# Optimization experiments

Hardware: AMD Instinct MI355X
Metric: run time of the kernel (lower is better)

## Reference

```python
import jax, jax.numpy as jnp
import numpy as np


def _orthogonal(key, n):
    a = jax.random.normal(key, (n, n), dtype=jnp.float32)
    q, r = jnp.linalg.qr(a)
    # sign correction as in torch.nn.init.orthogonal_
    q = q * jnp.sign(jnp.diag(r))
    return q


def setup_inputs() -> dict:
    key = jax.random.key(0)
    k_x, k_b, k_l = jax.random.split(key, 3)
    bs, seq_len, x_dim = 128, 2048, 256
    x_set = jax.random.normal(k_x, (bs, seq_len, x_dim), dtype=jnp.float32)
    B = _orthogonal(k_b, x_dim)
    Lam = _orthogonal(k_l, x_dim)
    return {"x_set": x_set, "B": B, "Lam": Lam}


def reference(x_set, B, Lam):
    # h_t = tanh(B @ x_t + Lambda @ h_{t-1}), h_0-input = 0
    # torch: bmm(B, x[:,T,None]) == x_t @ B.T for row-vector batch layout
    bs, seq_len, x_dim = x_set.shape

    def step(h, x_t):
        h_new = jnp.tanh(x_t @ B.T + h @ Lam.T)  # [bs, x_dim]
        return h_new, h_new

    h0 = jnp.zeros((bs, x_dim), dtype=x_set.dtype)
    _, hs = jax.lax.scan(step, h0, jnp.swapaxes(x_set, 0, 1))  # [T, bs, x_dim]
    return jnp.swapaxes(hs, 0, 1)  # [bs, T, x_dim]
```

## Files before the change

### kernel.cpp

```cpp
#include <hip/hip_runtime.h>

#define TT 2048
#define DD 256

typedef __fp16 half2_t __attribute__((ext_vector_type(2)));
typedef __fp16 half8_t __attribute__((ext_vector_type(8)));
typedef float f32x4_t __attribute__((ext_vector_type(4)));

static __device__ __forceinline__ float fdot2(half2_t a, half2_t b, float c) {
  return __builtin_amdgcn_fdot2(a, b, c, false);
}

static __device__ __forceinline__ float fast_tanh(float y) {
  float e = __builtin_amdgcn_exp2f(y * 2.885390081777927f);
  return 1.0f - 2.0f * __builtin_amdgcn_rcpf(e + 1.0f);
}

static __device__ __forceinline__ float dpp_xor1(float v) {
  return __builtin_bit_cast(float, __builtin_amdgcn_update_dpp(
      0, __builtin_bit_cast(int, v), 0xB1 , 0xF, 0xF, true));
}
static __device__ __forceinline__ float dpp_xor2(float v) {
  return __builtin_bit_cast(float, __builtin_amdgcn_update_dpp(
      0, __builtin_bit_cast(int, v), 0x4E , 0xF, 0xF, true));
}
static __device__ __forceinline__ float dpp_xor8(float v) {
  return __builtin_bit_cast(float, __builtin_amdgcn_update_dpp(
      0, __builtin_bit_cast(int, v), 0x128 , 0xF, 0xF, true));
}

#define BST 264
__global__ __launch_bounds__(256, 1) void rnn_u_gemm(
    const float* __restrict__ X, const float* __restrict__ Bm,
    float* __restrict__ U)
{
  extern __shared__ __fp16 bsh[];
  const int tid = threadIdx.x;

  {
    const float* br = Bm + tid * DD;
    __fp16* dst = bsh + tid * BST;
#pragma unroll
    for (int c = 0; c < 32; ++c) {
      float4 v0 = *(const float4*)(br + c * 8);
      float4 v1 = *(const float4*)(br + c * 8 + 4);
      uint4 w;
      w.x = __builtin_bit_cast(unsigned int, __builtin_amdgcn_cvt_pkrtz(v0.x, v0.y));
      w.y = __builtin_bit_cast(unsigned int, __builtin_amdgcn_cvt_pkrtz(v0.z, v0.w));
      w.z = __builtin_bit_cast(unsigned int, __builtin_amdgcn_cvt_pkrtz(v1.x, v1.y));
      w.w = __builtin_bit_cast(unsigned int, __builtin_amdgcn_cvt_pkrtz(v1.z, v1.w));
      *(uint4*)(dst + c * 8) = w;
    }
  }
  __syncthreads();

  const int wv = tid >> 6;
  const int l = tid & 63;
  const int l16 = l & 15;
  const int lk = l >> 4;
  const size_t tok0 = (size_t)blockIdx.x * 128 + wv * 32;

  f32x4_t acc[2][16];
#pragma unroll
  for (int m = 0; m < 2; ++m)
#pragma unroll
    for (int n = 0; n < 16; ++n)
      acc[m][n] = (f32x4_t){0.f, 0.f, 0.f, 0.f};

  const float* xA0 = X + (tok0 + l16) * DD + lk * 8;
  const float* xA1 = X + (tok0 + 16 + l16) * DD + lk * 8;

#pragma unroll
  for (int ks = 0; ks < 8; ++ks) {
    float4 a00 = *(const float4*)(xA0 + ks * 32);
    float4 a01 = *(const float4*)(xA0 + ks * 32 + 4);
    float4 a10 = *(const float4*)(xA1 + ks * 32);
    float4 a11 = *(const float4*)(xA1 + ks * 32 + 4);
    half2_t p0 = __builtin_amdgcn_cvt_pkrtz(a00.x, a00.y);
    half2_t p1 = __builtin_amdgcn_cvt_pkrtz(a00.z, a00.w);
    half2_t p2 = __builtin_amdgcn_cvt_pkrtz(a01.x, a01.y);
    half2_t p3 = __builtin_amdgcn_cvt_pkrtz(a01.z, a01.w);
    half2_t r0 = __builtin_amdgcn_cvt_pkrtz(a10.x, a10.y);
    half2_t r1 = __builtin_amdgcn_cvt_pkrtz(a10.z, a10.w);
    half2_t r2 = __builtin_amdgcn_cvt_pkrtz(a11.x, a11.y);
    half2_t r3 = __builtin_amdgcn_cvt_pkrtz(a11.z, a11.w);
    half8_t af0 = {p0[0], p0[1], p1[0], p1[1], p2[0], p2[1], p3[0], p3[1]};
    half8_t af1 = {r0[0], r0[1], r1[0], r1[1], r2[0], r2[1], r3[0], r3[1]};
#pragma unroll
    for (int n = 0; n < 16; ++n) {
      half8_t bf = *(const half8_t*)(bsh + (n * 16 + l16) * BST + ks * 32 + lk * 8);
      acc[0][n] = __builtin_amdgcn_mfma_f32_16x16x32_f16(af0, bf, acc[0][n], 0, 0, 0);
      acc[1][n] = __builtin_amdgcn_mfma_f32_16x16x32_f16(af1, bf, acc[1][n], 0, 0, 0);
    }
  }

#pragma unroll
  for (int m = 0; m < 2; ++m) {
    float* ub = U + (tok0 + m * 16 + lk * 4) * DD + l16;
#pragma unroll
    for (int n = 0; n < 16; ++n)
#pragma unroll
      for (int r = 0; r < 4; ++r)
        ub[(size_t)r * DD + n * 16] = acc[m][n][r];
  }
}

__global__ __launch_bounds__(512, 1) void rnn_scan(
    const float* __restrict__ Lm, float* outp )
{
  const int b = blockIdx.x;
  const int tid = threadIdx.x;
  const int wid = tid >> 6;
  const int lane = tid & 63;
  const int b0 = lane & 1, b1 = (lane >> 1) & 1, b3 = (lane >> 3) & 1;
  const int s = b0 | (b1 << 1) | (b3 << 2);
  const int s3 = s & 3;
  const int g = ((lane >> 2) & 1) | (((lane >> 4) & 3) << 1);
  const int G = (wid << 3) | g;
  const int jbase = G << 2;
  const int rmap = (b0 << 1) | b1;
  const int j_out = jbase + rmap;
  const bool wr = (b3 == 0);
  const bool s1b = (b0 != 0);
  const bool s2b = (b1 != 0);

  __shared__ __align__(16) __fp16 hbuf[2][DD];

  half2_t lamw[4][16];
#pragma unroll
  for (int r = 0; r < 4; ++r) {
    const float* lp = Lm + (jbase + r) * DD + s * 32;
#pragma unroll
    for (int q = 0; q < 8; ++q) {
      float4 v = *(const float4*)(lp + q * 4);
      lamw[r][2 * q]     = __builtin_amdgcn_cvt_pkrtz(v.x, v.y);
      lamw[r][2 * q + 1] = __builtin_amdgcn_cvt_pkrtz(v.z, v.w);
    }
  }

  const __fp16* hb0 = &hbuf[0][s * 32];
  const __fp16* hb1 = &hbuf[1][s * 32];
  const int o0 = 8 * (0 ^ s3), o1 = 8 * (1 ^ s3);
  const int o2 = 8 * (2 ^ s3), o3 = 8 * (3 ^ s3);
  const int posj = (j_out & ~24) | ((((j_out >> 3) & 3) ^ ((j_out >> 5) & 3)) << 3);
  __fp16* hw0p = &hbuf[0][posj];
  __fp16* hw1p = &hbuf[1][posj];

  const size_t obase = (size_t)b * (TT * DD) + j_out;

  if (tid < 128) ((unsigned int*)hbuf)[tid] = 0u;
  float up0 = outp[obase + 0 * DD];
  float up1 = outp[obase + 1 * DD];
  float up2 = outp[obase + 2 * DD];
  float up3 = outp[obase + 3 * DD];
  __syncthreads();

#define STEP(t, up, p)                                                         \
  {                                                                            \
    const __fp16* hbp = (p) ? hb1 : hb0;                                       \
    uint4 hv0 = *(const uint4*)(hbp + o0);                                     \
    uint4 hv1 = *(const uint4*)(hbp + o1);                                     \
    uint4 hv2 = *(const uint4*)(hbp + o2);                                     \
    uint4 hv3 = *(const uint4*)(hbp + o3);                                     \
    unsigned int hw[16] = {hv0.x, hv0.y, hv0.z, hv0.w,                         \
                           hv1.x, hv1.y, hv1.z, hv1.w,                         \
                           hv2.x, hv2.y, hv2.z, hv2.w,                         \
                           hv3.x, hv3.y, hv3.z, hv3.w};                        \
    float accv[4];                                                             \
    _Pragma("unroll")                                                          \
    for (int r = 0; r < 4; ++r) {                                              \
      float A = 0.f, Bc = 0.f;                                                 \
      _Pragma("unroll")                                                        \
      for (int w2 = 0; w2 < 8; ++w2) {                                         \
        A  = fdot2(lamw[r][2 * w2],     __builtin_bit_cast(half2_t, hw[2 * w2]),     A);  \
        Bc = fdot2(lamw[r][2 * w2 + 1], __builtin_bit_cast(half2_t, hw[2 * w2 + 1]), Bc); \
      }                                                                        \
      accv[r] = A + Bc;                                                        \
    }                                                                          \
             \
    float t0 = s1b ? accv[0] : accv[2], u0 = s1b ? accv[2] : accv[0];          \
    float t1 = s1b ? accv[1] : accv[3], u1 = s1b ? accv[3] : accv[1];          \
    float e0 = u0 + dpp_xor1(t0);                                              \
    float e1 = u1 + dpp_xor1(t1);                                              \
                               \
    float v0 = s2b ? e0 : e1, w0 = s2b ? e1 : e0;                              \
    float c0 = w0 + dpp_xor2(v0);                                              \
                                 \
    float pre = c0 + dpp_xor8(c0) + (up);                                      \
    float hn = fast_tanh(pre);                                                 \
    if (wr) {                                                                  \
      outp[obase + (size_t)(t) * DD] = hn;                                     \
      *((p) ? hw0p : hw1p) = (__fp16)hn;                 \
    }                                                                          \
    { int tn = (t) + 4; tn = tn > TT - 1 ? TT - 1 : tn;                        \
      up = outp[obase + (size_t)tn * DD]; }                                    \
    asm volatile("s_waitcnt lgkmcnt(0)" ::: "memory");                         \
    __builtin_amdgcn_s_barrier();                                              \
    asm volatile("" ::: "memory");                                             \
  }

  for (int t = 0; t < TT; t += 4) {
    STEP(t + 0, up0, 0)
    STEP(t + 1, up1, 1)
    STEP(t + 2, up2, 0)
    STEP(t + 3, up3, 1)
  }
#undef STEP
}

extern "C" void kernel_launch(void* const* d_in, const int* in_sizes, int n_in,
                              void* d_out, int out_size, void* d_ws, size_t ws_size,
                              hipStream_t stream) {
  const float* X  = (const float*)d_in[0];
  const float* Bm = (const float*)d_in[1];
  const float* Lm = (const float*)d_in[2];
  float* out = (float*)d_out;

  (void)hipFuncSetAttribute((const void*)rnn_u_gemm,
                            hipFuncAttributeMaxDynamicSharedMemorySize,
                            256 * BST * 2);
  hipLaunchKernelGGL(rnn_u_gemm, dim3(2048), dim3(256), 256 * BST * 2, stream,
                     X, Bm, out);
  hipLaunchKernelGGL(rnn_scan, dim3(128), dim3(512), 0, stream, Lm, out);
}
```

Baseline: 1.151 ms.

## Halve scan block to 256 threads with 16 rows per lane group

Restructures the recurrent scan so each block uses 4 waves instead of 8. Each 16-lane group now owns 16 output rows and each lane holds a 16-column slice of Lambda for all 16 rows (128 packed half2 registers). The cross-lane reduction becomes a four-stage DPP butterfly (xor1, xor2, xor7, xor8), and hidden values are written to LDS as packed pairs using a swizzled address. Fewer waves should make the per-step barrier cheaper and cut LDS read traffic, at the cost of more register pressure and more dot-product work per lane each step.

```diff
diff --git a/kernel.cpp b/kernel.cpp
--- a/kernel.cpp
+++ b/kernel.cpp
@@ -23,6 +23,10 @@
 static __device__ __forceinline__ float dpp_xor2(float v) {
   return __builtin_bit_cast(float, __builtin_amdgcn_update_dpp(
       0, __builtin_bit_cast(int, v), 0x4E , 0xF, 0xF, true));
+}
+static __device__ __forceinline__ float dpp_xor7(float v) {
+  return __builtin_bit_cast(float, __builtin_amdgcn_update_dpp(
+      0, __builtin_bit_cast(int, v), 0x141 , 0xF, 0xF, true));
 }
 static __device__ __forceinline__ float dpp_xor8(float v) {
   return __builtin_bit_cast(float, __builtin_amdgcn_update_dpp(
@@ -105,48 +109,40 @@
   }
 }
 
-__global__ __launch_bounds__(512, 1) void rnn_scan(
+__global__ __launch_bounds__(256, 1) void rnn_scan(
     const float* __restrict__ Lm, float* outp )
 {
-  const int b = blockIdx.x;
+  const int bb = blockIdx.x;
   const int tid = threadIdx.x;
   const int wid = tid >> 6;
   const int lane = tid & 63;
-  const int b0 = lane & 1, b1 = (lane >> 1) & 1, b3 = (lane >> 3) & 1;
-  const int s = b0 | (b1 << 1) | (b3 << 2);
-  const int s3 = s & 3;
-  const int g = ((lane >> 2) & 1) | (((lane >> 4) & 3) << 1);
-  const int G = (wid << 3) | g;
-  const int jbase = G << 2;
-  const int rmap = (b0 << 1) | b1;
+  const int b0 = lane & 1, b1 = (lane >> 1) & 1, b2 = (lane >> 2) & 1;
+  const int b3 = (lane >> 3) & 1, b4 = (lane >> 4) & 1, b5 = (lane >> 5) & 1;
+  const int s = lane & 15;
+  const int G = (wid << 2) | (b5 << 1) | b4;
+  const int jbase = G << 4;
+  const int rmap = (b0 << 3) ^ (b1 << 2) ^ (b2 ? 14 : 0) ^ b3;
   const int j_out = jbase + rmap;
-  const bool wr = (b3 == 0);
-  const bool s1b = (b0 != 0);
-  const bool s2b = (b1 != 0);
-
-  __shared__ __align__(16) __fp16 hbuf[2][DD];
-
-  half2_t lamw[4][16];
-#pragma unroll
-  for (int r = 0; r < 4; ++r) {
-    const float* lp = Lm + (jbase + r) * DD + s * 32;
-#pragma unroll
-    for (int q = 0; q < 8; ++q) {
-      float4 v = *(const float4*)(lp + q * 4);
-      lamw[r][2 * q]     = __builtin_amdgcn_cvt_pkrtz(v.x, v.y);
-      lamw[r][2 * q + 1] = __builtin_amdgcn_cvt_pkrtz(v.z, v.w);
+
+  __shared__ __align__(16) __fp16 hbuf[2 * DD];
+
+  half2_t lamw[16][8];
+#pragma unroll
+  for (int i = 0; i < 16; ++i) {
+    const float* lp = Lm + (jbase + (i ^ rmap)) * DD + s * 16;
+#pragma unroll
+    for (int c = 0; c < 4; ++c) {
+      float4 v = *(const float4*)(lp + c * 4);
+      lamw[i][2 * c]     = __builtin_amdgcn_cvt_pkrtz(v.x, v.y);
+      lamw[i][2 * c + 1] = __builtin_amdgcn_cvt_pkrtz(v.z, v.w);
     }
   }
 
-  const __fp16* hb0 = &hbuf[0][s * 32];
-  const __fp16* hb1 = &hbuf[1][s * 32];
-  const int o0 = 8 * (0 ^ s3), o1 = 8 * (1 ^ s3);
-  const int o2 = 8 * (2 ^ s3), o3 = 8 * (3 ^ s3);
-  const int posj = (j_out & ~24) | ((((j_out >> 3) & 3) ^ ((j_out >> 5) & 3)) << 3);
-  __fp16* hw0p = &hbuf[0][posj];
-  __fp16* hw1p = &hbuf[1][posj];
-
-  const size_t obase = (size_t)b * (TT * DD) + j_out;
+  const char* hrd = (const char*)hbuf + s * 16;
+  const int wbyte = ((b0 ^ b2) << 8) + (G << 4) + ((b1 ^ b2) << 3) + (b2 << 2);
+  char* hwr = (char*)hbuf + wbyte;
+
+  const size_t obase = (size_t)bb * (TT * DD) + j_out;
 
   if (tid < 128) ((unsigned int*)hbuf)[tid] = 0u;
   float up0 = outp[obase + 0 * DD];
@@ -157,40 +153,42 @@
 
 #define STEP(t, up, p)                                                         \
   {                                                                            \
-    const __fp16* hbp = (p) ? hb1 : hb0;                                       \
-    uint4 hv0 = *(const uint4*)(hbp + o0);                                     \
-    uint4 hv1 = *(const uint4*)(hbp + o1);                                     \
-    uint4 hv2 = *(const uint4*)(hbp + o2);                                     \
-    uint4 hv3 = *(const uint4*)(hbp + o3);                                     \
-    unsigned int hw[16] = {hv0.x, hv0.y, hv0.z, hv0.w,                         \
-                           hv1.x, hv1.y, hv1.z, hv1.w,                         \
-                           hv2.x, hv2.y, hv2.z, hv2.w,                         \
-                           hv3.x, hv3.y, hv3.z, hv3.w};                        \
-    float accv[4];                                                             \
+    uint4 hv0 = *(const uint4*)(hrd + (p) * 512);                              \
+    uint4 hv1 = *(const uint4*)(hrd + (p) * 512 + 256);                        \
+    unsigned int hd[8] = {hv0.x, hv0.y, hv0.z, hv0.w,                          \
+                          hv1.x, hv1.y, hv1.z, hv1.w};                         \
+    float acc[16];                                                             \
     _Pragma("unroll")                                                          \
-    for (int r = 0; r < 4; ++r) {                                              \
-      float A = 0.f, Bc = 0.f;                                                 \
+    for (int i = 0; i < 16; ++i) {                                             \
+      float a = 0.f;                                                           \
       _Pragma("unroll")                                                        \
-      for (int w2 = 0; w2 < 8; ++w2) {                                         \
-        A  = fdot2(lamw[r][2 * w2],     __builtin_bit_cast(half2_t, hw[2 * w2]),     A);  \
-        Bc = fdot2(lamw[r][2 * w2 + 1], __builtin_bit_cast(half2_t, hw[2 * w2 + 1]), Bc); \
-      }                                                                        \
-      accv[r] = A + Bc;                                                        \
+      for (int q = 0; q < 8; ++q)                                              \
+        a = fdot2(lamw[i][q], __builtin_bit_cast(half2_t, hd[q]), a);          \
+      acc[i] = a;                                                              \
     }                                                                          \
-             \
-    float t0 = s1b ? accv[0] : accv[2], u0 = s1b ? accv[2] : accv[0];          \
-    float t1 = s1b ? accv[1] : accv[3], u1 = s1b ? accv[3] : accv[1];          \
-    float e0 = u0 + dpp_xor1(t0);                                              \
-    float e1 = u1 + dpp_xor1(t1);                                              \
-                               \
-    float v0 = s2b ? e0 : e1, w0 = s2b ? e1 : e0;                              \
-    float c0 = w0 + dpp_xor2(v0);                                              \
-                                 \
-    float pre = c0 + dpp_xor8(c0) + (up);                                      \
+        \
+    float r0 = acc[0] + dpp_xor1(acc[8]);                                      \
+    float r1 = acc[1] + dpp_xor1(acc[9]);                                      \
+    float r2 = acc[2] + dpp_xor1(acc[10]);                                     \
+    float r3 = acc[3] + dpp_xor1(acc[11]);                                     \
+    float r4 = acc[4] + dpp_xor1(acc[12]);                                     \
+    float r5 = acc[5] + dpp_xor1(acc[13]);                                     \
+    float r6 = acc[6] + dpp_xor1(acc[14]);                                     \
+    float r7 = acc[7] + dpp_xor1(acc[15]);                                     \
+    float s0 = r0 + dpp_xor2(r4);                                              \
+    float s1 = r1 + dpp_xor2(r5);                                              \
+    float s2 = r2 + dpp_xor2(r6);                                              \
+    float s3 = r3 + dpp_xor2(r7);                                              \
+    float t0 = s0 + dpp_xor7(s2);                                              \
+    float t1 = s1 + dpp_xor7(s3);                                              \
+    float pre = t0 + dpp_xor8(t1) + (up);                                      \
     float hn = fast_tanh(pre);                                                 \
-    if (wr) {                                                                  \
-      outp[obase + (size_t)(t) * DD] = hn;                                     \
-      *((p) ? hw0p : hw1p) = (__fp16)hn;                 \
+    outp[obase + (size_t)(t) * DD] = hn;                                       \
+    float pn = dpp_xor8(hn);                 \
+    if (b3 == 0) {                                                             \
+      half2_t pk = __builtin_amdgcn_cvt_pkrtz(hn, pn);                         \
+      *(unsigned int*)(hwr + ((p) ^ 1) * 512) =                                \
+          __builtin_bit_cast(unsigned int, pk);                                \
     }                                                                          \
     { int tn = (t) + 4; tn = tn > TT - 1 ? TT - 1 : tn;                        \
       up = outp[obase + (size_t)tn * DD]; }                                    \
@@ -221,5 +219,5 @@
                             256 * BST * 2);
   hipLaunchKernelGGL(rnn_u_gemm, dim3(2048), dim3(256), 256 * BST * 2, stream,
                      X, Bm, out);
-  hipLaunchKernelGGL(rnn_scan, dim3(128), dim3(512), 0, stream, Lm, out);
-}
+  hipLaunchKernelGGL(rnn_scan, dim3(128), dim3(256), 0, stream, Lm, out);
+}
```

Result: faster. 1.009 ms (-12.4%).
